# Kernel tuning notes

Hardware: AMD Instinct MI355X
Metric: run time of the kernel (lower is better)

Reference implementation:

```python
import jax, jax.numpy as jnp
import numpy as np

LMAX = 4  # number of l blocks (lmax+1 in the original)
# segment ids mapping the L2 = sum(2l+1) = 16 spherical components to their l block
SEG = np.repeat(np.arange(LMAX), 2 * np.arange(LMAX) + 1)  # [16]
SEG_ONEHOT = np.eye(LMAX, dtype=np.float32)[SEG]  # [16, LMAX]


def setup_inputs() -> dict:
    key = jax.random.key(0)
    ks = jax.random.split(key, 10)
    b, m, f, k, L2 = 16, 64, 128, 64, 16
    def rnd(kk, shape, scale):
        return jax.random.normal(kk, shape, dtype=jnp.float32) * scale
    return {
        'x': rnd(ks[0], (b, m, f, L2), 1.0),
        'y': rnd(ks[1], (b, m, f, L2), 1.0),
        'wx0': rnd(ks[2], (k, f, f, LMAX), 1.0 / np.sqrt(f * f * LMAX)),
        'wy0': rnd(ks[3], (k, f, f, LMAX), 1.0 / np.sqrt(f * f * LMAX)),
        'wx_mlp': rnd(ks[4], (2, k, k), 1.0 / np.sqrt(k)),
        'bx_mlp': rnd(ks[5], (2, k, k), 0.02),
        'wy_mlp': rnd(ks[6], (2, k, k), 1.0 / np.sqrt(k)),
        'by_mlp': rnd(ks[7], (2, k, k), 0.02),
        'wxf': rnd(ks[8], (LMAX, f, k), 1.0 / np.sqrt(k)),
        'wyf': rnd(ks[9], (LMAX, f, k), 1.0 / np.sqrt(k)),
    }


def reference(x, y, wx0, wy0, wx_mlp, bx_mlp, wy_mlp, by_mlp, wxf, wyf):
    act = jax.nn.silu
    S = jnp.asarray(SEG_ONEHOT)  # [L2, lmax]
    # outer product of y and x features, segment-summed over each l block:
    # mix[b,m,fy,fx,l] = sum_c y[b,m,fy,c] * x[b,m,fx,c] * S[c,l]
    mix = jnp.einsum('bmfc,bmgc,cl->bmfgl', y, x, S)  # [b,m,f,f,lmax]
    mx = jnp.einsum('bmfgl,kfgl->bmk', mix, wx0)
    my = jnp.einsum('bmfgl,kfgl->bmk', mix, wy0)
    for i in range(wx_mlp.shape[0]):  # the n_mlp-1 used MLP stages
        mx = act(jnp.einsum('bmk,kl->bml', mx, wx_mlp[i]) + bx_mlp[i])
        my = act(jnp.einsum('bmk,kl->bml', my, wy_mlp[i]) + by_mlp[i])
    mx = act(jnp.einsum('bmk,lfk->bmfl', mx, wxf))  # [b,m,f,lmax]
    my = act(jnp.einsum('bmk,lfk->bmfl', my, wyf))
    # broadcast each l gate over its 2l+1 components (repeat == gather by SEG)
    seg = jnp.asarray(SEG)
    res = mx[..., seg] * x + my[..., seg] * y  # [b,m,f,L2]
    return res
```

## Files before the change

kernel.cpp:

```cpp
#include <hip/hip_runtime.h>
#include <stdint.h>


typedef __bf16 bf16x8 __attribute__((ext_vector_type(8)));
typedef float f32x4 __attribute__((ext_vector_type(4)));

__device__ __forceinline__ uint16_t f2b(float f) {
  uint32_t u = __float_as_uint(f);
  u += 0x7fffu + ((u >> 16) & 1u);
  return (uint16_t)(u >> 16);
}
__device__ __forceinline__ float b2f(uint16_t u) {
  return __uint_as_float((uint32_t)u << 16);
}
__device__ __forceinline__ uint32_t pk2(float a, float b) {
  return (uint32_t)f2b(a) | ((uint32_t)f2b(b) << 16);
}

#if __has_builtin(__builtin_amdgcn_fdot2_f32_bf16)
typedef __bf16 bf16x2 __attribute__((ext_vector_type(2)));
__device__ __forceinline__ float dot2b(uint32_t a, uint32_t b, float c) {
  union { uint32_t u; bf16x2 v; } ua, ub;
  ua.u = a; ub.u = b;
  return __builtin_amdgcn_fdot2_f32_bf16(ua.v, ub.v, c, false);
}
#else
__device__ __forceinline__ float dot2b(uint32_t a, uint32_t b, float c) {
  float a0 = __uint_as_float(a << 16), a1 = __uint_as_float(a & 0xffff0000u);
  float b0 = __uint_as_float(b << 16), b1 = __uint_as_float(b & 0xffff0000u);
  return c + a0 * b0 + a1 * b1;
}
#endif

#define LGKM_BAR() asm volatile("s_waitcnt lgkmcnt(0)\n\ts_barrier" ::: "memory")

__global__ __launch_bounds__(256) void wft_kernel(const float* __restrict__ wxf,
                                                  const float* __restrict__ wyf,
                                                  float* __restrict__ wfT) {
  int idx = blockIdx.x * 256 + threadIdx.x;
  int side = idx >> 15;
  int rem = idx & 32767;
  int k = rem >> 9;
  int l = (rem >> 7) & 3;
  int f = rem & 127;
  const float* src = side ? wyf : wxf;
  wfT[idx] = src[((size_t)l * 128 + f) * 64 + k];
}

__global__ __launch_bounds__(256, 3) void fused_gemm(
    const float* __restrict__ x, const float* __restrict__ y,
    const float* __restrict__ wx0, const float* __restrict__ wy0,
    uint16_t* __restrict__ Cpart) {
  __shared__ __align__(16) uint16_t smem[20480];
  const int seg[16] = {0,1,1,1,2,2,2,2,2,3,3,3,3,3,3,3};
  const int aoff0 = 0, aoff1 = 5120, boff0 = 10240, boff1 = 15360;

  int tid = threadIdx.x;
  int w = tid >> 6, lane = tid & 63;
  int g_id = blockIdx.x;
  int fb = g_id >> 3, fyg = g_id & 7;
  int FB = fb * 8;
  int fy0 = fyg * 16;
  int m0 = blockIdx.y * 128;
  int r = lane & 15, q = lane >> 4;
  int wm = w >> 1, wn = w & 1;
  int m_loc = tid & 127, half = tid >> 7;
  int n_row = tid >> 1, kc = tid & 1;

  const float* xrow = x + (size_t)(m0 + m_loc) * 2048 + (FB + half * 4) * 16;
  const float* yrow = y + (size_t)(m0 + m_loc) * 2048;
  const float* wrow = (n_row < 64) ? (wx0 + (size_t)n_row * 65536)
                                   : (wy0 + (size_t)(n_row - 64) * 65536);
  const float* wbase = wrow + FB * 4 + kc * 16;

  float4 Bv[4], Yv[4];
  auto issue = [&](int t) {
    const float* bp = wbase + (size_t)(fy0 + t) * 512;
    Bv[0] = *(const float4*)(bp);
    Bv[1] = *(const float4*)(bp + 4);
    Bv[2] = *(const float4*)(bp + 8);
    Bv[3] = *(const float4*)(bp + 12);
    const float* ypt = yrow + (size_t)(fy0 + t) * 16;
    Yv[0] = *(const float4*)(ypt);
    Yv[1] = *(const float4*)(ypt + 4);
    Yv[2] = *(const float4*)(ypt + 8);
    Yv[3] = *(const float4*)(ypt + 12);
  };

  float4 xv[16];
#pragma unroll
  for (int p = 0; p < 16; ++p) xv[p] = *(const float4*)(xrow + p * 4);
  issue(0);
  uint32_t xr[32];
#pragma unroll
  for (int fxp = 0; fxp < 4; ++fxp)
#pragma unroll
    for (int cc = 0; cc < 4; ++cc) {
      float4 v = xv[fxp * 4 + cc];
      xr[fxp * 8 + cc * 2 + 0] = pk2(v.x, v.y);
      xr[fxp * 8 + cc * 2 + 1] = pk2(v.z, v.w);
    }

  f32x4 zero = {0.f, 0.f, 0.f, 0.f};
  f32x4 acc[4][4];
#pragma unroll
  for (int i = 0; i < 4; ++i)
#pragma unroll
    for (int j = 0; j < 4; ++j) acc[i][j] = zero;

  auto stage = [&](int ao, int bo) {
    uint32_t bq[8];
#pragma unroll
    for (int p = 0; p < 4; ++p) {
      bq[2 * p]     = pk2(Bv[p].x, Bv[p].y);
      bq[2 * p + 1] = pk2(Bv[p].z, Bv[p].w);
    }
    uint16_t* bd = &smem[bo + n_row * 40 + kc * 16];
    *(uint4*)bd       = make_uint4(bq[0], bq[1], bq[2], bq[3]);
    *(uint4*)(bd + 8) = make_uint4(bq[4], bq[5], bq[6], bq[7]);
    uint32_t yq[8];
    yq[0] = pk2(Yv[0].x, Yv[0].y); yq[1] = pk2(Yv[0].z, Yv[0].w);
    yq[2] = pk2(Yv[1].x, Yv[1].y); yq[3] = pk2(Yv[1].z, Yv[1].w);
    yq[4] = pk2(Yv[2].x, Yv[2].y); yq[5] = pk2(Yv[2].z, Yv[2].w);
    yq[6] = pk2(Yv[3].x, Yv[3].y); yq[7] = pk2(Yv[3].z, Yv[3].w);
    uint32_t yl0 = yq[0] & 0xffffu, yh0 = yq[0] & 0xffff0000u;
    uint32_t yl4 = yq[4] & 0xffffu, yh4 = yq[4] & 0xffff0000u;
    float gg[16];
#pragma unroll
    for (int fxp = 0; fxp < 4; ++fxp) {
      const uint32_t* xp = xr + fxp * 8;
      gg[fxp * 4 + 0] = dot2b(xp[0], yl0, 0.f);
      gg[fxp * 4 + 1] = dot2b(xp[1], yq[1], dot2b(xp[0], yh0, 0.f));
      gg[fxp * 4 + 2] = dot2b(xp[4], yl4,
                          dot2b(xp[3], yq[3], dot2b(xp[2], yq[2], 0.f)));
      gg[fxp * 4 + 3] = dot2b(xp[7], yq[7], dot2b(xp[6], yq[6],
                          dot2b(xp[5], yq[5], dot2b(xp[4], yh4, 0.f))));
    }
    uint32_t go[8];
#pragma unroll
    for (int p = 0; p < 8; ++p) go[p] = pk2(gg[2 * p], gg[2 * p + 1]);
    uint16_t* ad = &smem[ao + m_loc * 40 + half * 16];
    *(uint4*)ad       = make_uint4(go[0], go[1], go[2], go[3]);
    *(uint4*)(ad + 8) = make_uint4(go[4], go[5], go[6], go[7]);
  };

  stage(aoff0, boff0);
  issue(1);
  __syncthreads();

  for (int t = 0; t < 16; ++t) {
    int cur = t & 1;
    int aoc = cur ? aoff1 : aoff0, bocur = cur ? boff1 : boff0;
    int aon = cur ? aoff0 : aoff1, bonxt = cur ? boff0 : boff1;
    if (t < 15) stage(aon, bonxt);
    if (t < 14) issue(t + 2);
    bf16x8 a[4], b[4];
#pragma unroll
    for (int i = 0; i < 4; ++i)
      a[i] = *(const bf16x8*)&smem[aoc + (wm * 64 + i * 16 + r) * 40 + q * 8];
#pragma unroll
    for (int j = 0; j < 4; ++j)
      b[j] = *(const bf16x8*)&smem[bocur + (wn * 64 + j * 16 + r) * 40 + q * 8];
#pragma unroll
    for (int i = 0; i < 4; ++i)
#pragma unroll
      for (int j = 0; j < 4; ++j)
        acc[i][j] = __builtin_amdgcn_mfma_f32_16x16x32_bf16(a[i], b[j], acc[i][j], 0, 0, 0);
    LGKM_BAR();
  }

  __syncthreads();
#pragma unroll
  for (int i = 0; i < 4; ++i)
#pragma unroll
    for (int j = 0; j < 4; ++j)
#pragma unroll
      for (int reg = 0; reg < 4; ++reg) {
        int mm = wm * 64 + i * 16 + q * 4 + reg;
        int nn = wn * 64 + j * 16 + r;
        smem[mm * 128 + nn] = f2b(acc[i][j][reg]);
      }
  __syncthreads();
  {
    int row = tid >> 1, ch = tid & 1;
    const uint16_t* csrc = &smem[row * 128 + ch * 64];
    uint16_t* cdst = Cpart + (size_t)g_id * 131072 +
                     (size_t)(m0 + row) * 128 + ch * 64;
#pragma unroll
    for (int kkk = 0; kkk < 8; ++kkk)
      *(uint4*)(cdst + kkk * 8) = *(const uint4*)(csrc + kkk * 8);
  }
}

__global__ __launch_bounds__(256) void finish_kernel(
    const float* __restrict__ x, const float* __restrict__ y,
    const float* __restrict__ wx_mlp, const float* __restrict__ bx_mlp,
    const float* __restrict__ wy_mlp, const float* __restrict__ by_mlp,
    const float* __restrict__ wfT,
    const uint16_t* __restrict__ Cpart, float* __restrict__ out) {
  const int seg[16] = {0,1,1,1,2,2,2,2,2,3,3,3,3,3,3,3};
  __shared__ float sred[256];
  __shared__ float sm[128];
  __shared__ float sg[2][128][4];
  int t = threadIdx.x;
  int bm = blockIdx.x;
  int mi = bm & 63;

  {
    int col = t & 127, hh = t >> 7;
    float s = 0.f;
#pragma unroll 8
    for (int sp = hh * 64; sp < hh * 64 + 64; ++sp)
      s += b2f(Cpart[(size_t)sp * 131072 + (size_t)bm * 128 + col]);
    sred[t] = s;
  }
  __syncthreads();
  if (t < 128) sm[t] = sred[t] + sred[t + 128];
  __syncthreads();

  for (int st = 0; st < 2; ++st) {
    float v = 0.f;
    if (t < 128) {
      int side = t >> 6, j = t & 63;
      const float* wmlp = side ? wy_mlp : wx_mlp;
      const float* bmlp = side ? by_mlp : bx_mlp;
      const float* mv = sm + side * 64;
#pragma unroll 8
      for (int k = 0; k < 64; ++k)
        v += mv[k] * wmlp[(st * 64 + k) * 64 + j];
      v += bmlp[(st * 64 + mi) * 64 + j];
      v = v / (1.f + __expf(-v));
    }
    __syncthreads();
    if (t < 128) sm[t] = v;
    __syncthreads();
  }

  {
    int side = t >> 7, f = t & 127;
    const float* base = wfT + side * 32768;
    const float* mv = sm + side * 64;
    float gg[4] = {0.f, 0.f, 0.f, 0.f};
#pragma unroll 8
    for (int k = 0; k < 64; ++k) {
      float m2 = mv[k];
#pragma unroll
      for (int l = 0; l < 4; ++l)
        gg[l] += m2 * base[(k * 4 + l) * 128 + f];
    }
#pragma unroll
    for (int l = 0; l < 4; ++l)
      sg[side][f][l] = gg[l] / (1.f + __expf(-gg[l]));
  }
  __syncthreads();

  {
    int f = t >> 1, half = t & 1;
    size_t base = ((size_t)bm * 128 + f) * 16 + half * 8;
    float4 xa = *(const float4*)(x + base), xb4 = *(const float4*)(x + base + 4);
    float4 ya = *(const float4*)(y + base), yb4 = *(const float4*)(y + base + 4);
    float xv[8] = {xa.x, xa.y, xa.z, xa.w, xb4.x, xb4.y, xb4.z, xb4.w};
    float yv[8] = {ya.x, ya.y, ya.z, ya.w, yb4.x, yb4.y, yb4.z, yb4.w};
    float o[8];
#pragma unroll
    for (int ii = 0; ii < 8; ++ii) {
      int c = half * 8 + ii;
      o[ii] = sg[0][f][seg[c]] * xv[ii] + sg[1][f][seg[c]] * yv[ii];
    }
    *(float4*)(out + base)     = make_float4(o[0], o[1], o[2], o[3]);
    *(float4*)(out + base + 4) = make_float4(o[4], o[5], o[6], o[7]);
  }
}

extern "C" void kernel_launch(void* const* d_in, const int* in_sizes, int n_in,
                              void* d_out, int out_size, void* d_ws, size_t ws_size,
                              hipStream_t stream) {
  const float* x      = (const float*)d_in[0];
  const float* y      = (const float*)d_in[1];
  const float* wx0    = (const float*)d_in[2];
  const float* wy0    = (const float*)d_in[3];
  const float* wx_mlp = (const float*)d_in[4];
  const float* bx_mlp = (const float*)d_in[5];
  const float* wy_mlp = (const float*)d_in[6];
  const float* by_mlp = (const float*)d_in[7];
  const float* wxf    = (const float*)d_in[8];
  const float* wyf    = (const float*)d_in[9];
  float* out = (float*)d_out;

  uint16_t* Cpart = (uint16_t*)d_ws;
  float*    wfT   = (float*)((char*)d_ws + (size_t)33554432);

  wft_kernel<<<256, 256, 0, stream>>>(wxf, wyf, wfT);
  fused_gemm<<<dim3(128, 8), 256, 0, stream>>>(x, y, wx0, wy0, Cpart);
  finish_kernel<<<1024, 256, 0, stream>>>(x, y, wx_mlp, bx_mlp, wy_mlp, by_mlp,
                                          wfT, Cpart, out);
}
```

Baseline: 194.2 us.

## Preconvert weights to bf16 and hold B fragments in registers per wave

Adds a prepass that converts wx0/wy0 to bf16 once, merged with the wf transpose kernel. The GEMM now has each wave own 32 rows and load the whole 128-wide B operand straight from global into registers as MFMA fragments. This drops the shared-memory B staging and the block-wide barriers, and the A tile becomes a per-wave shared slot. y is also truncated to bf16 with a byte permute instead of rounding. In exchange the kernel spends more registers, every wave reloads the same B data, and the extra pass over the 32MB of weights costs memory traffic.

```diff
diff --git a/kernel.cpp b/kernel.cpp
--- a/kernel.cpp
+++ b/kernel.cpp
@@ -16,6 +16,15 @@
 __device__ __forceinline__ uint32_t pk2(float a, float b) {
   return (uint32_t)f2b(a) | ((uint32_t)f2b(b) << 16);
 }
+#if __has_builtin(__builtin_amdgcn_perm)
+__device__ __forceinline__ uint32_t pkt(uint32_t lo, uint32_t hi) {
+  return __builtin_amdgcn_perm(hi, lo, 0x07060302u);
+}
+#else
+__device__ __forceinline__ uint32_t pkt(uint32_t lo, uint32_t hi) {
+  return (lo >> 16) | (hi & 0xffff0000u);
+}
+#endif
 
 #if __has_builtin(__builtin_amdgcn_fdot2_f32_bf16)
 typedef __bf16 bf16x2 __attribute__((ext_vector_type(2)));
@@ -32,65 +41,60 @@
 }
 #endif
 
-#define LGKM_BAR() asm volatile("s_waitcnt lgkmcnt(0)\n\ts_barrier" ::: "memory")
-
-__global__ __launch_bounds__(256) void wft_kernel(const float* __restrict__ wxf,
-                                                  const float* __restrict__ wyf,
-                                                  float* __restrict__ wfT) {
-  int idx = blockIdx.x * 256 + threadIdx.x;
-  int side = idx >> 15;
-  int rem = idx & 32767;
-  int k = rem >> 9;
-  int l = (rem >> 7) & 3;
-  int f = rem & 127;
-  const float* src = side ? wyf : wxf;
-  wfT[idx] = src[((size_t)l * 128 + f) * 64 + k];
-}
-
-__global__ __launch_bounds__(256, 3) void fused_gemm(
+__global__ __launch_bounds__(256) void convert_kernel(
+    const float* __restrict__ wx0, const float* __restrict__ wy0,
+    const float* __restrict__ wxf, const float* __restrict__ wyf,
+    uint16_t* __restrict__ Wb, float* __restrict__ wfT) {
+  if (blockIdx.x < 4096) {
+    size_t i = ((size_t)blockIdx.x * 256 + threadIdx.x) * 8;
+    const float* s = (i < 4194304) ? (wx0 + i) : (wy0 + (i - 4194304));
+    float4 v0 = *(const float4*)s;
+    float4 v1 = *(const float4*)(s + 4);
+    *(uint4*)(Wb + i) = make_uint4(pk2(v0.x, v0.y), pk2(v0.z, v0.w),
+                                   pk2(v1.x, v1.y), pk2(v1.z, v1.w));
+  } else {
+    int base = (blockIdx.x - 4096) * 2048 + threadIdx.x * 8;
+#pragma unroll
+    for (int ii = 0; ii < 8; ++ii) {
+      int idx = base + ii;
+      int side = idx >> 15, rem = idx & 32767;
+      int k = rem >> 9, l = (rem >> 7) & 3, f = rem & 127;
+      const float* src = side ? wyf : wxf;
+      wfT[idx] = src[((size_t)l * 128 + f) * 64 + k];
+    }
+  }
+}
+
+__global__ __launch_bounds__(256) void fused_gemm(
     const float* __restrict__ x, const float* __restrict__ y,
-    const float* __restrict__ wx0, const float* __restrict__ wy0,
-    uint16_t* __restrict__ Cpart) {
-  __shared__ __align__(16) uint16_t smem[20480];
-  const int seg[16] = {0,1,1,1,2,2,2,2,2,3,3,3,3,3,3,3};
-  const int aoff0 = 0, aoff1 = 5120, boff0 = 10240, boff1 = 15360;
+    const uint16_t* __restrict__ Wb, uint16_t* __restrict__ Cpart) {
+  __shared__ __align__(16) uint16_t smem[16384];
 
   int tid = threadIdx.x;
-  int w = tid >> 6, lane = tid & 63;
+  int wid = tid >> 6, lane = tid & 63;
   int g_id = blockIdx.x;
   int fb = g_id >> 3, fyg = g_id & 7;
-  int FB = fb * 8;
-  int fy0 = fyg * 16;
+  int FB = fb * 8, fy0 = fyg * 16;
   int m0 = blockIdx.y * 128;
   int r = lane & 15, q = lane >> 4;
-  int wm = w >> 1, wn = w & 1;
-  int m_loc = tid & 127, half = tid >> 7;
-  int n_row = tid >> 1, kc = tid & 1;
-
-  const float* xrow = x + (size_t)(m0 + m_loc) * 2048 + (FB + half * 4) * 16;
-  const float* yrow = y + (size_t)(m0 + m_loc) * 2048;
-  const float* wrow = (n_row < 64) ? (wx0 + (size_t)n_row * 65536)
-                                   : (wy0 + (size_t)(n_row - 64) * 65536);
-  const float* wbase = wrow + FB * 4 + kc * 16;
-
-  float4 Bv[4], Yv[4];
-  auto issue = [&](int t) {
-    const float* bp = wbase + (size_t)(fy0 + t) * 512;
-    Bv[0] = *(const float4*)(bp);
-    Bv[1] = *(const float4*)(bp + 4);
-    Bv[2] = *(const float4*)(bp + 8);
-    Bv[3] = *(const float4*)(bp + 12);
-    const float* ypt = yrow + (size_t)(fy0 + t) * 16;
-    Yv[0] = *(const float4*)(ypt);
-    Yv[1] = *(const float4*)(ypt + 4);
-    Yv[2] = *(const float4*)(ypt + 8);
-    Yv[3] = *(const float4*)(ypt + 12);
-  };
+  int mw = lane & 31, halfw = lane >> 5;
+  int mrow = m0 + wid * 32 + mw;
+
+  const float* xrow = x + (size_t)mrow * 2048 + (FB + halfw * 4) * 16;
+  const float* yrow = y + (size_t)mrow * 2048 + fy0 * 16;
+  const uint16_t* wlane = Wb + (size_t)r * 65536 + (size_t)fy0 * 512 + FB * 4 + q * 8;
 
   float4 xv[16];
 #pragma unroll
   for (int p = 0; p < 16; ++p) xv[p] = *(const float4*)(xrow + p * 4);
-  issue(0);
+  uint4 Wp[8];
+#pragma unroll
+  for (int j = 0; j < 8; ++j)
+    Wp[j] = *(const uint4*)(wlane + (size_t)j * 1048576);
+  float4 Yv[4];
+#pragma unroll
+  for (int p = 0; p < 4; ++p) Yv[p] = *(const float4*)(yrow + p * 4);
+
   uint32_t xr[32];
 #pragma unroll
   for (int fxp = 0; fxp < 4; ++fxp)
@@ -102,27 +106,29 @@
     }
 
   f32x4 zero = {0.f, 0.f, 0.f, 0.f};
-  f32x4 acc[4][4];
-#pragma unroll
-  for (int i = 0; i < 4; ++i)
-#pragma unroll
-    for (int j = 0; j < 4; ++j) acc[i][j] = zero;
-
-  auto stage = [&](int ao, int bo) {
-    uint32_t bq[8];
-#pragma unroll
-    for (int p = 0; p < 4; ++p) {
-      bq[2 * p]     = pk2(Bv[p].x, Bv[p].y);
-      bq[2 * p + 1] = pk2(Bv[p].z, Bv[p].w);
-    }
-    uint16_t* bd = &smem[bo + n_row * 40 + kc * 16];
-    *(uint4*)bd       = make_uint4(bq[0], bq[1], bq[2], bq[3]);
-    *(uint4*)(bd + 8) = make_uint4(bq[4], bq[5], bq[6], bq[7]);
+  f32x4 acc[2][8];
+#pragma unroll
+  for (int i = 0; i < 2; ++i)
+#pragma unroll
+    for (int j = 0; j < 8; ++j) acc[i][j] = zero;
+
+  int slot = wid * 2560;
+
+  for (int t = 0; t < 16; ++t) {
     uint32_t yq[8];
-    yq[0] = pk2(Yv[0].x, Yv[0].y); yq[1] = pk2(Yv[0].z, Yv[0].w);
-    yq[2] = pk2(Yv[1].x, Yv[1].y); yq[3] = pk2(Yv[1].z, Yv[1].w);
-    yq[4] = pk2(Yv[2].x, Yv[2].y); yq[5] = pk2(Yv[2].z, Yv[2].w);
-    yq[6] = pk2(Yv[3].x, Yv[3].y); yq[7] = pk2(Yv[3].z, Yv[3].w);
+    yq[0] = pkt(__float_as_uint(Yv[0].x), __float_as_uint(Yv[0].y));
+    yq[1] = pkt(__float_as_uint(Yv[0].z), __float_as_uint(Yv[0].w));
+    yq[2] = pkt(__float_as_uint(Yv[1].x), __float_as_uint(Yv[1].y));
+    yq[3] = pkt(__float_as_uint(Yv[1].z), __float_as_uint(Yv[1].w));
+    yq[4] = pkt(__float_as_uint(Yv[2].x), __float_as_uint(Yv[2].y));
+    yq[5] = pkt(__float_as_uint(Yv[2].z), __float_as_uint(Yv[2].w));
+    yq[6] = pkt(__float_as_uint(Yv[3].x), __float_as_uint(Yv[3].y));
+    yq[7] = pkt(__float_as_uint(Yv[3].z), __float_as_uint(Yv[3].w));
+    if (t < 15) {
+      const float* yp = yrow + (size_t)(t + 1) * 16;
+#pragma unroll
+      for (int p = 0; p < 4; ++p) Yv[p] = *(const float4*)(yp + p * 4);
+    }
     uint32_t yl0 = yq[0] & 0xffffu, yh0 = yq[0] & 0xffff0000u;
     uint32_t yl4 = yq[4] & 0xffffu, yh4 = yq[4] & 0xffff0000u;
     float gg[16];
@@ -136,48 +142,37 @@
       gg[fxp * 4 + 3] = dot2b(xp[7], yq[7], dot2b(xp[6], yq[6],
                           dot2b(xp[5], yq[5], dot2b(xp[4], yh4, 0.f))));
     }
-    uint32_t go[8];
-#pragma unroll
-    for (int p = 0; p < 8; ++p) go[p] = pk2(gg[2 * p], gg[2 * p + 1]);
-    uint16_t* ad = &smem[ao + m_loc * 40 + half * 16];
-    *(uint4*)ad       = make_uint4(go[0], go[1], go[2], go[3]);
-    *(uint4*)(ad + 8) = make_uint4(go[4], go[5], go[6], go[7]);
-  };
-
-  stage(aoff0, boff0);
-  issue(1);
-  __syncthreads();
-
-  for (int t = 0; t < 16; ++t) {
-    int cur = t & 1;
-    int aoc = cur ? aoff1 : aoff0, bocur = cur ? boff1 : boff0;
-    int aon = cur ? aoff0 : aoff1, bonxt = cur ? boff0 : boff1;
-    if (t < 15) stage(aon, bonxt);
-    if (t < 14) issue(t + 2);
-    bf16x8 a[4], b[4];
-#pragma unroll
-    for (int i = 0; i < 4; ++i)
-      a[i] = *(const bf16x8*)&smem[aoc + (wm * 64 + i * 16 + r) * 40 + q * 8];
-#pragma unroll
-    for (int j = 0; j < 4; ++j)
-      b[j] = *(const bf16x8*)&smem[bocur + (wn * 64 + j * 16 + r) * 40 + q * 8];
-#pragma unroll
-    for (int i = 0; i < 4; ++i)
-#pragma unroll
-      for (int j = 0; j < 4; ++j)
-        acc[i][j] = __builtin_amdgcn_mfma_f32_16x16x32_bf16(a[i], b[j], acc[i][j], 0, 0, 0);
-    LGKM_BAR();
-  }
-
-  __syncthreads();
-#pragma unroll
-  for (int i = 0; i < 4; ++i)
-#pragma unroll
-    for (int j = 0; j < 4; ++j)
+    int ab = slot + (t & 1) * 1280;
+    {
+      uint32_t go[8];
+#pragma unroll
+      for (int p = 0; p < 8; ++p) go[p] = pk2(gg[2 * p], gg[2 * p + 1]);
+      uint16_t* ad = &smem[ab + mw * 40 + halfw * 16];
+      *(uint4*)ad       = make_uint4(go[0], go[1], go[2], go[3]);
+      *(uint4*)(ad + 8) = make_uint4(go[4], go[5], go[6], go[7]);
+    }
+    bf16x8 a0 = *(const bf16x8*)&smem[ab + r * 40 + q * 8];
+    bf16x8 a1 = *(const bf16x8*)&smem[ab + (16 + r) * 40 + q * 8];
+#pragma unroll
+    for (int j = 0; j < 8; ++j) {
+      union { uint4 u; bf16x8 v; } bb;
+      bb.u = Wp[j];
+      acc[0][j] = __builtin_amdgcn_mfma_f32_16x16x32_bf16(a0, bb.v, acc[0][j], 0, 0, 0);
+      acc[1][j] = __builtin_amdgcn_mfma_f32_16x16x32_bf16(a1, bb.v, acc[1][j], 0, 0, 0);
+      if (t < 15)
+        Wp[j] = *(const uint4*)(wlane + (size_t)j * 1048576 + (size_t)(t + 1) * 512);
+    }
+  }
+
+  __syncthreads();
+#pragma unroll
+  for (int i = 0; i < 2; ++i)
+#pragma unroll
+    for (int j = 0; j < 8; ++j)
 #pragma unroll
       for (int reg = 0; reg < 4; ++reg) {
-        int mm = wm * 64 + i * 16 + q * 4 + reg;
-        int nn = wn * 64 + j * 16 + r;
+        int mm = wid * 32 + i * 16 + q * 4 + reg;
+        int nn = j * 16 + r;
         smem[mm * 128 + nn] = f2b(acc[i][j][reg]);
       }
   __syncthreads();
@@ -287,11 +282,12 @@
   const float* wyf    = (const float*)d_in[9];
   float* out = (float*)d_out;
 
-  uint16_t* Cpart = (uint16_t*)d_ws;
-  float*    wfT   = (float*)((char*)d_ws + (size_t)33554432);
-
-  wft_kernel<<<256, 256, 0, stream>>>(wxf, wyf, wfT);
-  fused_gemm<<<dim3(128, 8), 256, 0, stream>>>(x, y, wx0, wy0, Cpart);
+  uint16_t* Wb    = (uint16_t*)d_ws;
+  uint16_t* Cpart = (uint16_t*)((char*)d_ws + (size_t)16777216);
+  float*    wfT   = (float*)((char*)d_ws + (size_t)50331648);
+
+  convert_kernel<<<4128, 256, 0, stream>>>(wx0, wy0, wxf, wyf, Wb, wfT);
+  fused_gemm<<<dim3(128, 8), 256, 0, stream>>>(x, y, Wb, Cpart);
   finish_kernel<<<1024, 256, 0, stream>>>(x, y, wx_mlp, bx_mlp, wy_mlp, by_mlp,
                                           wfT, Cpart, out);
 }
```

Measured after the change: 227.3 us. +17.0%, slower.
